# Kernel optimization log

Hardware: AMD Instinct MI355X
Metric: run time of the kernel (lower is better)

Reference implementation:

```python
import jax, jax.numpy as jnp
import numpy as np

D = 384        # model dim
H = 6          # heads
HD = 64        # head dim (inner_dim = H*HD = 384)
DEPTH = 12
P = 16         # patch size
G = 14         # grid side (224/16)
NP = G * G     # 196 patches
NC = 1000
B = 64
DFF = 4 * D
SCALE = HD ** -0.5
EPS = 1e-5


def _ln(x, w, b):
    m = x.mean(-1, keepdims=True)
    v = ((x - m) ** 2).mean(-1, keepdims=True)
    return (x - m) * jax.lax.rsqrt(v + EPS) * w + b


def setup_inputs() -> dict:
    key = jax.random.key(0)
    ks = jax.random.split(key, 16)
    s = 0.02
    inp = {
        "x": jax.random.normal(ks[0], (B, 3, 224, 224), jnp.float32),
        # patch embedding conv as matmul: weight [3*P*P, D]
        "W_patch": jax.random.normal(ks[1], (3 * P * P, D), jnp.float32) * s,
        "b_patch": jnp.zeros((D,), jnp.float32),
        "ln0_w": jnp.ones((D,), jnp.float32),
        "ln0_b": jnp.zeros((D,), jnp.float32),
        "pos_emb": jax.random.normal(ks[2], (1, NP + 1, D), jnp.float32) * s,
        "cls_token": jax.random.normal(ks[3], (1, D), jnp.float32),
        # per-block params stacked over depth
        "ln1_w": jnp.ones((DEPTH, D), jnp.float32),
        "ln1_b": jnp.zeros((DEPTH, D), jnp.float32),
        "Wq": jax.random.normal(ks[4], (DEPTH, D, H * HD), jnp.float32) * s,
        "Wkv": jax.random.normal(ks[5], (DEPTH, D, 2 * H * HD), jnp.float32) * s,
        "Wo": jax.random.normal(ks[6], (DEPTH, H * HD, D), jnp.float32) * s,
        "bo": jnp.zeros((DEPTH, D), jnp.float32),
        "ln2_w": jnp.ones((DEPTH, D), jnp.float32),
        "ln2_b": jnp.zeros((DEPTH, D), jnp.float32),
        "W1": jax.random.normal(ks[7], (DEPTH, D, DFF), jnp.float32) * s,
        "b1": jnp.zeros((DEPTH, DFF), jnp.float32),
        "W2": jax.random.normal(ks[8], (DEPTH, DFF, D), jnp.float32) * s,
        "b2": jnp.zeros((DEPTH, D), jnp.float32),
        "lnf_w": jnp.ones((D,), jnp.float32),
        "lnf_b": jnp.zeros((D,), jnp.float32),
        "Whead": jax.random.normal(ks[9], (D, NC), jnp.float32) * s,
        "bhead": jnp.zeros((NC,), jnp.float32),
    }
    return inp


def reference(x, W_patch, b_patch, ln0_w, ln0_b, pos_emb, cls_token,
              ln1_w, ln1_b, Wq, Wkv, Wo, bo, ln2_w, ln2_b,
              W1, b1, W2, b2, lnf_w, lnf_b, Whead, bhead):
    b = x.shape[0]
    # patch embed: Conv2d(3, D, P, stride=P) == extract patches + matmul
    patches = x.reshape(b, 3, G, P, G, P).transpose(0, 2, 4, 1, 3, 5).reshape(b, NP, 3 * P * P)
    h = patches @ W_patch + b_patch                     # [b, NP, D]
    h = _ln(h, ln0_w, ln0_b)
    cls = jnp.broadcast_to(cls_token[None], (b, 1, D))
    h = jnp.concatenate([cls, h], axis=1) + pos_emb     # [b, NP+1, D]
    n = NP + 1
    for d in range(DEPTH):
        # self-attention with pre-LN, residual
        a = _ln(h, ln1_w[d], ln1_b[d])
        q = (a @ Wq[d]).reshape(b, n, H, HD).transpose(0, 2, 1, 3)
        kv = a @ Wkv[d]
        k = kv[..., : H * HD].reshape(b, n, H, HD).transpose(0, 2, 1, 3)
        v = kv[..., H * HD:].reshape(b, n, H, HD).transpose(0, 2, 1, 3)
        sim = jnp.einsum('bhid,bhjd->bhij', q, k) * SCALE
        attn = jax.nn.softmax(sim, axis=-1)
        o = jnp.einsum('bhij,bhjd->bhid', attn, v)
        o = o.transpose(0, 2, 1, 3).reshape(b, n, H * HD)
        h = h + o @ Wo[d] + bo[d]
        # MLP with pre-LN, residual, exact GELU
        m = _ln(h, ln2_w[d], ln2_b[d])
        m = jax.nn.gelu(m @ W1[d] + b1[d], approximate=False)
        h = h + m @ W2[d] + b2[d]
    cls_out = h[:, 0, :]
    logits = _ln(cls_out, lnf_w, lnf_b) @ Whead + bhead
    return logits
```

## Files before the change

### kernel.cpp

```cpp
#include <hip/hip_runtime.h>


typedef unsigned short u16;
typedef __attribute__((ext_vector_type(8))) short short8;
typedef __attribute__((ext_vector_type(4))) float f32x4;
typedef __attribute__((ext_vector_type(4))) unsigned short u16x4;
typedef __attribute__((ext_vector_type(2))) unsigned short u16x2;

#define D_      384
#define NH      6
#define DEPTH_  12
#define NP_     196
#define NT_     197
#define B_      64
#define DFF_    1536
#define M_REAL  (B_*NT_)
#define M_PAD   12672
#define M_PATCH (B_*NP_)

__device__ __forceinline__ float bf2f(u16 u){
  unsigned int i = ((unsigned int)u) << 16;
  return __builtin_bit_cast(float, i);
}
__device__ __forceinline__ u16 f2bf(float f){
  unsigned int i = __builtin_bit_cast(unsigned int, f);
  i = (i + 0x7FFFu + ((i >> 16) & 1u)) >> 16;
  return (u16)i;
}

#define GLOAD_LDS16(g, l) __builtin_amdgcn_global_load_lds( \
    (const __attribute__((address_space(1))) void*)(g),      \
    (__attribute__((address_space(3))) void*)(l), 16, 0, 0)

#define MFMA_BF16(a, b, c) __builtin_amdgcn_mfma_f32_16x16x32_bf16((a), (b), (c), 0, 0, 0)

__global__ __launch_bounds__(256) void transpose_cvt(const float* __restrict__ src,
                                                     u16* __restrict__ dst, int K, int N,
                                                     size_t sstride, size_t dstride)
{
  __shared__ float tile[32][33];
  src += blockIdx.z * sstride;
  dst += blockIdx.z * dstride;
  int tx = threadIdx.x, ty = threadIdx.y;
  int n0 = blockIdx.x * 32, k0 = blockIdx.y * 32;
#pragma unroll
  for (int i = 0; i < 4; ++i)
    tile[ty + i*8][tx] = src[(size_t)(k0 + ty + i*8) * N + n0 + tx];
  __syncthreads();
#pragma unroll
  for (int i = 0; i < 4; ++i)
    dst[(size_t)(n0 + ty + i*8) * K + k0 + tx] = f2bf(tile[tx][ty + i*8]);
}

__global__ __launch_bounds__(256) void patch_extract(const float* __restrict__ x,
                                                     u16* __restrict__ patches)
{
  int r = blockIdx.x;
  int b = r / NP_, p = r % NP_;
  int gy = p / 14, gx = p % 14;
  int t = threadIdx.x;
  int py = t >> 4, px = t & 15;
#pragma unroll
  for (int c = 0; c < 3; ++c){
    float v = x[(((size_t)b*3 + c)*224 + gy*16 + py)*224 + gx*16 + px];
    patches[(size_t)r*768 + c*256 + t] = f2bf(v);
  }
}

template<int MODE, int BM, int BN>
__global__ __launch_bounds__(256) void gemm_k(const u16* __restrict__ A,
                                              const u16* __restrict__ Bt,
                                              const float* __restrict__ bias,
                                              u16* __restrict__ outb,
                                              float* __restrict__ outf,
                                              int N, int K, int nbx)
{
  constexpr int MI = BM/32;
  constexpr int NJ = BN/32;
  constexpr int L  = BM/64 + BN/64;
  __shared__ u16 As[3*BM*32];
  __shared__ u16 Bs[3*BN*32];
  int tid = threadIdx.x;
  int w = tid >> 6, lane = tid & 63;

  int nwg = gridDim.x;
  int q = nwg >> 3, r = nwg & 7;
  int xcd = blockIdx.x & 7, slot = blockIdx.x >> 3;
  int wgid = (xcd < r ? xcd*(q+1) : r*(q+1) + (xcd - r)*q) + slot;
  int m0 = (wgid / nbx) * BM;
  int n0 = (wgid % nbx) * BN;
  int wr = w >> 1, wc = w & 1;

  f32x4 acc[MI][NJ];
#pragma unroll
  for (int i = 0; i < MI; ++i)
#pragma unroll
    for (int j = 0; j < NJ; ++j) acc[i][j] = (f32x4){0.f,0.f,0.f,0.f};

  int srow = lane >> 2;
  int skc  = ((lane & 3) ^ (srow & 3)) * 8;
  const u16* Ag = A  + (size_t)(m0 + w*16 + srow) * K + skc;
  const u16* Bg = Bt + (size_t)(n0 + w*16 + srow) * K + skc;

  int fr  = lane & 15;
  int fsw = ((lane >> 4) ^ (lane & 3)) << 3;

  auto stage = [&](int bi, int kt){
    u16* Ad = As + bi*(BM*32) + (w*16)*32;
    u16* Bd = Bs + bi*(BN*32) + (w*16)*32;
#pragma unroll
    for (int c = 0; c < BM/64; ++c)
      GLOAD_LDS16(Ag + (size_t)(c*64)*K + kt, Ad + c*64*32);
#pragma unroll
    for (int c = 0; c < BN/64; ++c)
      GLOAD_LDS16(Bg + (size_t)(c*64)*K + kt, Bd + c*64*32);
  };
  auto compute = [&](int bi){
    const u16* Ab = As + bi*(BM*32);
    const u16* Bb = Bs + bi*(BN*32);
    short8 af[MI], bfr[NJ];
#pragma unroll
    for (int i = 0; i < MI; ++i)
      af[i]  = *(const short8*)&Ab[(wr*(BM/2) + i*16 + fr)*32 + fsw];
#pragma unroll
    for (int j = 0; j < NJ; ++j)
      bfr[j] = *(const short8*)&Bb[(wc*(BN/2) + j*16 + fr)*32 + fsw];
#pragma unroll
    for (int i = 0; i < MI; ++i)
#pragma unroll
      for (int j = 0; j < NJ; ++j)
        acc[i][j] = MFMA_BF16(af[i], bfr[j], acc[i][j]);
  };

  int nk = K >> 5;
  stage(0, 0);
  stage(1, 32);
  int bi = 0;
  for (int t = 0; t < nk - 1; ++t){
    __builtin_amdgcn_sched_barrier(0);
    if constexpr (L == 2) asm volatile("s_waitcnt vmcnt(2)" ::: "memory");
    else                  asm volatile("s_waitcnt vmcnt(3)" ::: "memory");
    __builtin_amdgcn_s_barrier();
    asm volatile("" ::: "memory");
    compute(bi);
    if (t + 2 < nk){
      int bs = bi + 2; if (bs >= 3) bs -= 3;
      stage(bs, (t + 2) * 32);
    }
    bi = (bi == 2) ? 0 : bi + 1;
  }
  __builtin_amdgcn_sched_barrier(0);
  asm volatile("s_waitcnt vmcnt(0)" ::: "memory");
  __builtin_amdgcn_s_barrier();
  asm volatile("" ::: "memory");
  compute(bi);

  int cr = (lane >> 4) << 2;
  int cc = lane & 15;
#pragma unroll
  for (int j = 0; j < NJ; ++j){
    int c = n0 + wc*(BN/2) + j*16 + cc;
    float bv = bias ? bias[c] : 0.f;
#pragma unroll
    for (int i = 0; i < MI; ++i){
      int rbase = m0 + wr*(BM/2) + i*16 + cr;
#pragma unroll
      for (int e = 0; e < 4; ++e){
        float v = acc[i][j][e] + bv;
        size_t idx = (size_t)(rbase + e) * N + c;
        if (MODE == 0)      outb[idx] = f2bf(v);
        else if (MODE == 1) outf[idx] += v;
        else {
          float g = 0.5f * v * (1.f + erff(v * 0.70710678118654752f));
          outb[idx] = f2bf(g);
        }
      }
    }
  }
}

__global__ __launch_bounds__(256) void ln_rows(const float* __restrict__ in,
                                               const float* __restrict__ gw,
                                               const float* __restrict__ gb,
                                               u16* __restrict__ out, int rows)
{
  int m = blockIdx.x * 4 + (threadIdx.x >> 6);
  int lane = threadIdx.x & 63;
  if (m >= rows) return;
  const float* r = in + (size_t)m * D_;
  float4 v0 = *(const float4*)(r + lane*4);
  float2 v1 = *(const float2*)(r + 256 + lane*2);
  float sum = v0.x+v0.y+v0.z+v0.w+v1.x+v1.y;
  float sq  = v0.x*v0.x+v0.y*v0.y+v0.z*v0.z+v0.w*v0.w+v1.x*v1.x+v1.y*v1.y;
#pragma unroll
  for (int d = 1; d < 64; d <<= 1){ sum += __shfl_xor(sum, d); sq += __shfl_xor(sq, d); }
  float mean = sum * (1.f/D_);
  float rs = rsqrtf(sq*(1.f/D_) - mean*mean + 1e-5f);
  float4 w0 = *(const float4*)(gw + lane*4);
  float2 w1 = *(const float2*)(gw + 256 + lane*2);
  float4 b0 = *(const float4*)(gb + lane*4);
  float2 b1v= *(const float2*)(gb + 256 + lane*2);
  u16x4 o4 = { f2bf((v0.x-mean)*rs*w0.x + b0.x), f2bf((v0.y-mean)*rs*w0.y + b0.y),
               f2bf((v0.z-mean)*rs*w0.z + b0.z), f2bf((v0.w-mean)*rs*w0.w + b0.w) };
  u16x2 o2 = { f2bf((v1.x-mean)*rs*w1.x + b1v.x), f2bf((v1.y-mean)*rs*w1.y + b1v.y) };
  *(u16x4*)(out + (size_t)m*D_ + lane*4) = o4;
  *(u16x2*)(out + (size_t)m*D_ + 256 + lane*2) = o2;
}

__global__ __launch_bounds__(256) void assemble_h(const u16* __restrict__ pe,
                                                  const float* __restrict__ gw,
                                                  const float* __restrict__ gb,
                                                  const float* __restrict__ pos,
                                                  const float* __restrict__ cls,
                                                  float* __restrict__ h)
{
  int m = blockIdx.x * 4 + (threadIdx.x >> 6);
  int lane = threadIdx.x & 63;
  if (m >= M_PAD) return;
  float* ho = h + (size_t)m * D_;
  if (m >= M_REAL){
    float4 z = {0.f,0.f,0.f,0.f};
    *(float4*)(ho + lane*4) = z;
    float2 z2 = {0.f,0.f};
    *(float2*)(ho + 256 + lane*2) = z2;
    return;
  }
  int b = m / NT_, t = m % NT_;
  const float* pr = pos + (size_t)t * D_;
  float4 p0 = *(const float4*)(pr + lane*4);
  float2 p1 = *(const float2*)(pr + 256 + lane*2);
  if (t == 0){
    float4 c0 = *(const float4*)(cls + lane*4);
    float2 c1 = *(const float2*)(cls + 256 + lane*2);
    float4 r0 = {c0.x+p0.x, c0.y+p0.y, c0.z+p0.z, c0.w+p0.w};
    float2 r1 = {c1.x+p1.x, c1.y+p1.y};
    *(float4*)(ho + lane*4) = r0;
    *(float2*)(ho + 256 + lane*2) = r1;
  } else {
    const u16* per = pe + (size_t)(b*NP_ + (t-1)) * D_;
    u16x4 a0 = *(const u16x4*)(per + lane*4);
    u16x2 a1 = *(const u16x2*)(per + 256 + lane*2);
    float x0=bf2f(a0.x), x1=bf2f(a0.y), x2=bf2f(a0.z), x3=bf2f(a0.w), x4=bf2f(a1.x), x5=bf2f(a1.y);
    float sum = x0+x1+x2+x3+x4+x5;
    float sq  = x0*x0+x1*x1+x2*x2+x3*x3+x4*x4+x5*x5;
#pragma unroll
    for (int d = 1; d < 64; d <<= 1){ sum += __shfl_xor(sum, d); sq += __shfl_xor(sq, d); }
    float mean = sum * (1.f/D_);
    float rs = rsqrtf(sq*(1.f/D_) - mean*mean + 1e-5f);
    float4 w0 = *(const float4*)(gw + lane*4);
    float2 w1 = *(const float2*)(gw + 256 + lane*2);
    float4 b0 = *(const float4*)(gb + lane*4);
    float2 b1v= *(const float2*)(gb + 256 + lane*2);
    float4 r0 = { (x0-mean)*rs*w0.x + b0.x + p0.x, (x1-mean)*rs*w0.y + b0.y + p0.y,
                  (x2-mean)*rs*w0.z + b0.z + p0.z, (x3-mean)*rs*w0.w + b0.w + p0.w };
    float2 r1 = { (x4-mean)*rs*w1.x + b1v.x + p1.x, (x5-mean)*rs*w1.y + b1v.y + p1.y };
    *(float4*)(ho + lane*4) = r0;
    *(float2*)(ho + 256 + lane*2) = r1;
  }
}

__global__ __launch_bounds__(256) void attn_k(const u16* __restrict__ qkv,
                                              u16* __restrict__ o)
{
  __shared__ u16 Ks[208*72];
  __shared__ u16 Vt[64*232];
  __shared__ u16 Ps[4][16*40];
  int bh = blockIdx.x;
  int b = bh / NH, hh = bh % NH;
  int tid = threadIdx.x, w = tid >> 6, lane = tid & 63;
  const u16* kbase = qkv + (size_t)b*NT_*1152 + 384 + hh*64;
  const u16* vbase = kbase + 384;

  int jr = tid >> 3, col = (tid & 7) * 8;
#pragma unroll
  for (int it = 0; it < 7; ++it){
    int j = it*32 + jr;
    if (j < 208){
      uint4 val = {0u,0u,0u,0u};
      if (j < 197) val = *(const uint4*)(kbase + (size_t)j*1152 + col);
      *(uint4*)&Ks[j*72 + col] = val;
    }
  }
#pragma unroll
  for (int it = 0; it < 7; ++it){
    int j = it*32 + jr;
    union { uint4 v; u16 s[8]; } u;
    u.v.x = 0u; u.v.y = 0u; u.v.z = 0u; u.v.w = 0u;
    if (j < 197) u.v = *(const uint4*)(vbase + (size_t)j*1152 + col);
#pragma unroll
    for (int e = 0; e < 8; ++e) Vt[(size_t)(col+e)*232 + j] = u.s[e];
  }
  __syncthreads();

  u16* myP = Ps[w];
  int fr = lane & 15, fk = lane >> 4;

  for (int qt = w; qt < 13; qt += 4){
    const u16* qrow = qkv + (size_t)(b*NT_ + qt*16 + fr)*1152 + hh*64 + fk*8;
    short8 aq0 = *(const short8*)qrow;
    short8 aq1 = *(const short8*)(qrow + 32);

    f32x4 s[13];
#pragma unroll
    for (int jt = 0; jt < 13; ++jt){
      const u16* kr = &Ks[(jt*16 + fr)*72 + fk*8];
      short8 bk0 = *(const short8*)kr;
      short8 bk1 = *(const short8*)(kr + 32);
      f32x4 z = {0.f,0.f,0.f,0.f};
      z = MFMA_BF16(aq0, bk0, z);
      z = MFMA_BF16(aq1, bk1, z);
      s[jt] = z;
    }

#pragma unroll
    for (int e = 0; e < 4; ++e){
      float mx = -1e30f;
#pragma unroll
      for (int jt = 0; jt < 13; ++jt){
        int cj = jt*16 + fr;
        float v = (cj < NT_) ? s[jt][e]*0.125f : -1e30f;
        s[jt][e] = v;
        mx = fmaxf(mx, v);
      }
#pragma unroll
      for (int d = 1; d < 16; d <<= 1) mx = fmaxf(mx, __shfl_xor(mx, d));
      float su = 0.f;
#pragma unroll
      for (int jt = 0; jt < 13; ++jt){
        float p = __expf(s[jt][e] - mx);
        s[jt][e] = p; su += p;
      }
#pragma unroll
      for (int d = 1; d < 16; d <<= 1) su += __shfl_xor(su, d);
      float ri = 1.f / su;
#pragma unroll
      for (int jt = 0; jt < 13; ++jt) s[jt][e] *= ri;
    }

    f32x4 oacc[4];
#pragma unroll
    for (int dt = 0; dt < 4; ++dt) oacc[dt] = (f32x4){0.f,0.f,0.f,0.f};
#pragma unroll
    for (int jc = 0; jc < 7; ++jc){
#pragma unroll
      for (int jtl = 0; jtl < 2; ++jtl){
        int jt = jc*2 + jtl;
#pragma unroll
        for (int e = 0; e < 4; ++e){
          u16 pv = 0;
          if (jt < 13) pv = f2bf(s[jt][e]);
          myP[(fk*4 + e)*40 + jtl*16 + fr] = pv;
        }
      }
      asm volatile("s_waitcnt lgkmcnt(0)" ::: "memory");
      short8 pa = *(const short8*)&myP[fr*40 + fk*8];
#pragma unroll
      for (int dt = 0; dt < 4; ++dt){
        short8 bv = *(const short8*)&Vt[(size_t)(dt*16 + fr)*232 + jc*32 + fk*8];
        oacc[dt] = MFMA_BF16(pa, bv, oacc[dt]);
      }
    }

#pragma unroll
    for (int dt = 0; dt < 4; ++dt)
#pragma unroll
      for (int e = 0; e < 4; ++e){
        int t = qt*16 + fk*4 + e;
        if (t < NT_)
          o[(size_t)(b*NT_ + t)*384 + hh*64 + dt*16 + fr] = f2bf(oacc[dt][e]);
      }
  }
}

__global__ __launch_bounds__(256) void head_k(const float* __restrict__ h,
                                              const float* __restrict__ lw,
                                              const float* __restrict__ lb,
                                              const float* __restrict__ Wh,
                                              const float* __restrict__ bh,
                                              float* __restrict__ out)
{
  __shared__ float sn[D_];
  __shared__ float red[2][4];
  int b = blockIdx.x;
  int tid = threadIdx.x;
  const float* r = h + (size_t)b * NT_ * D_;
  float x0 = r[tid];
  float x1 = (tid < 128) ? r[256 + tid] : 0.f;
  float sum = x0 + x1;
  float sq  = x0*x0 + x1*x1;
  int lane = tid & 63, w = tid >> 6;
#pragma unroll
  for (int d = 1; d < 64; d <<= 1){ sum += __shfl_xor(sum, d); sq += __shfl_xor(sq, d); }
  if (lane == 0){ red[0][w] = sum; red[1][w] = sq; }
  __syncthreads();
  sum = red[0][0]+red[0][1]+red[0][2]+red[0][3];
  sq  = red[1][0]+red[1][1]+red[1][2]+red[1][3];
  float mean = sum * (1.f/D_);
  float rs = rsqrtf(sq*(1.f/D_) - mean*mean + 1e-5f);
  sn[tid] = (x0-mean)*rs*lw[tid] + lb[tid];
  if (tid < 128) sn[256+tid] = (x1-mean)*rs*lw[256+tid] + lb[256+tid];
  __syncthreads();
  int n = blockIdx.y * 256 + tid;
  if (n < 1000){
    float acc = bh[n];
#pragma unroll 4
    for (int k = 0; k < D_; ++k) acc += sn[k] * Wh[(size_t)k*1000 + n];
    out[(size_t)b*1000 + n] = acc;
  }
}

extern "C" void kernel_launch(void* const* d_in, const int* in_sizes, int n_in,
                              void* d_out, int out_size, void* d_ws, size_t ws_size,
                              hipStream_t stream)
{
  (void)in_sizes; (void)n_in; (void)out_size; (void)ws_size;
  const float* x_in    = (const float*)d_in[0];
  const float* W_patch = (const float*)d_in[1];
  const float* b_patch = (const float*)d_in[2];
  const float* ln0_w   = (const float*)d_in[3];
  const float* ln0_b   = (const float*)d_in[4];
  const float* pos_emb = (const float*)d_in[5];
  const float* cls_tok = (const float*)d_in[6];
  const float* ln1_w   = (const float*)d_in[7];
  const float* ln1_b   = (const float*)d_in[8];
  const float* Wq      = (const float*)d_in[9];
  const float* Wkv     = (const float*)d_in[10];
  const float* Wo      = (const float*)d_in[11];
  const float* bo      = (const float*)d_in[12];
  const float* ln2_w   = (const float*)d_in[13];
  const float* ln2_b   = (const float*)d_in[14];
  const float* W1      = (const float*)d_in[15];
  const float* b1      = (const float*)d_in[16];
  const float* W2      = (const float*)d_in[17];
  const float* b2      = (const float*)d_in[18];
  const float* lnf_w   = (const float*)d_in[19];
  const float* lnf_b   = (const float*)d_in[20];
  const float* Whead   = (const float*)d_in[21];
  const float* bhead   = (const float*)d_in[22];

  char* ws = (char*)d_ws;
  size_t off = 0;
  auto nxt = [&](size_t bytes)->char* {
    char* p = ws + off;
    off += (bytes + 255) & ~(size_t)255;
    return p;
  };
  u16*   g_buf   = (u16*)  nxt((size_t)M_PAD * DFF_ * 2);
  float* hbuf    = (float*)nxt((size_t)M_PAD * D_ * 4);
  u16*   abuf    = (u16*)  nxt((size_t)M_PAD * D_ * 2);
  u16*   qkvbuf  = (u16*)  nxt((size_t)M_PAD * 1152 * 2);
  u16*   obuf    = (u16*)  nxt((size_t)M_PAD * D_ * 2);
  u16*   wT      = (u16*)  nxt((size_t)21528576 * 2);

  u16* patches = g_buf;
  u16* pebuf   = abuf;
  u16* wpT   = wT;
  u16* wqkvT = wpT   + 294912;
  u16* woT   = wqkvT + 12*442368;
  u16* w1T   = woT   + 12*147456;
  u16* w2T   = w1T   + 12*589824;

  dim3 tpb(32, 8);
  transpose_cvt<<<dim3(12, 24, 1),  tpb, 0, stream>>>(W_patch, wpT, 768, 384, 0, 0);
  transpose_cvt<<<dim3(12, 12, 12), tpb, 0, stream>>>(Wq,  wqkvT,            384, 384,
                                                      (size_t)384*384, (size_t)1152*384);
  transpose_cvt<<<dim3(24, 12, 12), tpb, 0, stream>>>(Wkv, wqkvT + 384*384,  384, 768,
                                                      (size_t)384*768, (size_t)1152*384);
  transpose_cvt<<<dim3(12, 12, 12), tpb, 0, stream>>>(Wo,  woT, 384, 384,
                                                      (size_t)384*384, (size_t)384*384);
  transpose_cvt<<<dim3(48, 12, 12), tpb, 0, stream>>>(W1,  w1T, 384, 1536,
                                                      (size_t)384*1536, (size_t)384*1536);
  transpose_cvt<<<dim3(12, 48, 12), tpb, 0, stream>>>(W2,  w2T, 1536, 384,
                                                      (size_t)1536*384, (size_t)1536*384);

  patch_extract<<<M_PATCH, 256, 0, stream>>>(x_in, patches);
  gemm_k<0,64,64><<<6*(M_PATCH/64), 256, 0, stream>>>(patches, wpT, b_patch, pebuf, nullptr, 384, 768, 6);
  assemble_h<<<M_PAD/4, 256, 0, stream>>>(pebuf, ln0_w, ln0_b, pos_emb, cls_tok, hbuf);

  for (int d = 0; d < DEPTH_; ++d){
    ln_rows<<<M_PAD/4, 256, 0, stream>>>(hbuf, ln1_w + d*384, ln1_b + d*384, abuf, M_PAD);
    gemm_k<0,64,128><<<9*(M_PAD/64), 256, 0, stream>>>(abuf, wqkvT + (size_t)d*442368, nullptr, qkvbuf, nullptr, 1152, 384, 9);
    attn_k<<<B_*NH, 256, 0, stream>>>(qkvbuf, obuf);
    gemm_k<1,64,64><<<6*(M_PAD/64), 256, 0, stream>>>(obuf, woT + (size_t)d*147456, bo + d*384, nullptr, hbuf, 384, 384, 6);
    ln_rows<<<M_PAD/4, 256, 0, stream>>>(hbuf, ln2_w + d*384, ln2_b + d*384, abuf, M_PAD);
    gemm_k<2,64,128><<<12*(M_PAD/64), 256, 0, stream>>>(abuf, w1T + (size_t)d*589824, b1 + d*1536, g_buf, nullptr, 1536, 384, 12);
    gemm_k<1,64,64><<<6*(M_PAD/64), 256, 0, stream>>>(g_buf, w2T + (size_t)d*589824, b2 + d*384, nullptr, hbuf, 384, 1536, 6);
  }

  head_k<<<dim3(B_, 4), 256, 0, stream>>>(hbuf, lnf_w, lnf_b, Whead, bhead, (float*)d_out);
}
```

Measured before the change: 1.989 ms.

## Enlarge GEMM tiles, add split-K with atomics, run classifier head through MFMA GEMM

All transformer GEMMs move to 128x128 tiles, and the two residual-add GEMMs (Wo and W2) split K across two blockIdx.y slices that accumulate into the fp32 residual with atomic adds. The bias is added only by the first slice. The patch-embedding GEMM widens to 64x128. The scalar head kernel is replaced by an LN on the CLS rows plus a bf16 MFMA GEMM against a padded, transposed head weight. Larger tiles cut redundant operand loads and split-K restores block count on the narrow-N GEMMs. In exchange, atomics make the summation order nondeterministic and the head now rounds to bf16.

```diff
diff --git a/kernel.cpp b/kernel.cpp
--- a/kernel.cpp
+++ b/kernel.cpp
@@ -36,6 +36,7 @@
 
 __global__ __launch_bounds__(256) void transpose_cvt(const float* __restrict__ src,
                                                      u16* __restrict__ dst, int K, int N,
+                                                     int Nsrc,
                                                      size_t sstride, size_t dstride)
 {
   __shared__ float tile[32][33];
@@ -44,8 +45,11 @@
   int tx = threadIdx.x, ty = threadIdx.y;
   int n0 = blockIdx.x * 32, k0 = blockIdx.y * 32;
 #pragma unroll
-  for (int i = 0; i < 4; ++i)
-    tile[ty + i*8][tx] = src[(size_t)(k0 + ty + i*8) * N + n0 + tx];
+  for (int i = 0; i < 4; ++i){
+    float v = 0.f;
+    if (n0 + tx < Nsrc) v = src[(size_t)(k0 + ty + i*8) * Nsrc + n0 + tx];
+    tile[ty + i*8][tx] = v;
+  }
   __syncthreads();
 #pragma unroll
   for (int i = 0; i < 4; ++i)
@@ -67,7 +71,7 @@
   }
 }
 
-template<int MODE, int BM, int BN>
+template<int MODE, int BM, int BN, int KS>
 __global__ __launch_bounds__(256) void gemm_k(const u16* __restrict__ A,
                                               const u16* __restrict__ Bt,
                                               const float* __restrict__ bias,
@@ -89,6 +93,9 @@
   int wgid = (xcd < r ? xcd*(q+1) : r*(q+1) + (xcd - r)*q) + slot;
   int m0 = (wgid / nbx) * BM;
   int n0 = (wgid % nbx) * BN;
+  int kz = (KS > 1) ? blockIdx.y : 0;
+  int Kl = K / KS;
+  int koff = kz * Kl;
   int wr = w >> 1, wc = w & 1;
 
   f32x4 acc[MI][NJ];
@@ -99,8 +106,8 @@
 
   int srow = lane >> 2;
   int skc  = ((lane & 3) ^ (srow & 3)) * 8;
-  const u16* Ag = A  + (size_t)(m0 + w*16 + srow) * K + skc;
-  const u16* Bg = Bt + (size_t)(n0 + w*16 + srow) * K + skc;
+  const u16* Ag = A  + (size_t)(m0 + w*16 + srow) * K + koff + skc;
+  const u16* Bg = Bt + (size_t)(n0 + w*16 + srow) * K + koff + skc;
 
   int fr  = lane & 15;
   int fsw = ((lane >> 4) ^ (lane & 3)) << 3;
@@ -132,14 +139,15 @@
         acc[i][j] = MFMA_BF16(af[i], bfr[j], acc[i][j]);
   };
 
-  int nk = K >> 5;
+  int nk = Kl >> 5;
   stage(0, 0);
   stage(1, 32);
   int bi = 0;
   for (int t = 0; t < nk - 1; ++t){
     __builtin_amdgcn_sched_barrier(0);
-    if constexpr (L == 2) asm volatile("s_waitcnt vmcnt(2)" ::: "memory");
-    else                  asm volatile("s_waitcnt vmcnt(3)" ::: "memory");
+    if constexpr (L == 2)      asm volatile("s_waitcnt vmcnt(2)" ::: "memory");
+    else if constexpr (L == 3) asm volatile("s_waitcnt vmcnt(3)" ::: "memory");
+    else                       asm volatile("s_waitcnt vmcnt(4)" ::: "memory");
     __builtin_amdgcn_s_barrier();
     asm volatile("" ::: "memory");
     compute(bi);
@@ -160,7 +168,7 @@
 #pragma unroll
   for (int j = 0; j < NJ; ++j){
     int c = n0 + wc*(BN/2) + j*16 + cc;
-    float bv = bias ? bias[c] : 0.f;
+    float bv = (bias && kz == 0) ? bias[c] : 0.f;
 #pragma unroll
     for (int i = 0; i < MI; ++i){
       int rbase = m0 + wr*(BM/2) + i*16 + cr;
@@ -169,10 +177,12 @@
         float v = acc[i][j][e] + bv;
         size_t idx = (size_t)(rbase + e) * N + c;
         if (MODE == 0)      outb[idx] = f2bf(v);
-        else if (MODE == 1) outf[idx] += v;
-        else {
+        else if (MODE == 1) unsafeAtomicAdd(&outf[idx], v);
+        else if (MODE == 2) {
           float g = 0.5f * v * (1.f + erff(v * 0.70710678118654752f));
           outb[idx] = f2bf(g);
+        } else {
+          if (c < N) outf[idx] = v;
         }
       }
     }
@@ -182,12 +192,13 @@
 __global__ __launch_bounds__(256) void ln_rows(const float* __restrict__ in,
                                                const float* __restrict__ gw,
                                                const float* __restrict__ gb,
-                                               u16* __restrict__ out, int rows)
+                                               u16* __restrict__ out, int rows,
+                                               size_t rstride)
 {
   int m = blockIdx.x * 4 + (threadIdx.x >> 6);
   int lane = threadIdx.x & 63;
   if (m >= rows) return;
-  const float* r = in + (size_t)m * D_;
+  const float* r = in + (size_t)m * rstride;
   float4 v0 = *(const float4*)(r + lane*4);
   float2 v1 = *(const float2*)(r + 256 + lane*2);
   float sum = v0.x+v0.y+v0.z+v0.w+v1.x+v1.y;
@@ -369,43 +380,6 @@
         if (t < NT_)
           o[(size_t)(b*NT_ + t)*384 + hh*64 + dt*16 + fr] = f2bf(oacc[dt][e]);
       }
-  }
-}
-
-__global__ __launch_bounds__(256) void head_k(const float* __restrict__ h,
-                                              const float* __restrict__ lw,
-                                              const float* __restrict__ lb,
-                                              const float* __restrict__ Wh,
-                                              const float* __restrict__ bh,
-                                              float* __restrict__ out)
-{
-  __shared__ float sn[D_];
-  __shared__ float red[2][4];
-  int b = blockIdx.x;
-  int tid = threadIdx.x;
-  const float* r = h + (size_t)b * NT_ * D_;
-  float x0 = r[tid];
-  float x1 = (tid < 128) ? r[256 + tid] : 0.f;
-  float sum = x0 + x1;
-  float sq  = x0*x0 + x1*x1;
-  int lane = tid & 63, w = tid >> 6;
-#pragma unroll
-  for (int d = 1; d < 64; d <<= 1){ sum += __shfl_xor(sum, d); sq += __shfl_xor(sq, d); }
-  if (lane == 0){ red[0][w] = sum; red[1][w] = sq; }
-  __syncthreads();
-  sum = red[0][0]+red[0][1]+red[0][2]+red[0][3];
-  sq  = red[1][0]+red[1][1]+red[1][2]+red[1][3];
-  float mean = sum * (1.f/D_);
-  float rs = rsqrtf(sq*(1.f/D_) - mean*mean + 1e-5f);
-  sn[tid] = (x0-mean)*rs*lw[tid] + lb[tid];
-  if (tid < 128) sn[256+tid] = (x1-mean)*rs*lw[256+tid] + lb[256+tid];
-  __syncthreads();
-  int n = blockIdx.y * 256 + tid;
-  if (n < 1000){
-    float acc = bh[n];
-#pragma unroll 4
-    for (int k = 0; k < D_; ++k) acc += sn[k] * Wh[(size_t)k*1000 + n];
-    out[(size_t)b*1000 + n] = acc;
   }
 }
 
@@ -450,6 +424,8 @@
   u16*   abuf    = (u16*)  nxt((size_t)M_PAD * D_ * 2);
   u16*   qkvbuf  = (u16*)  nxt((size_t)M_PAD * 1152 * 2);
   u16*   obuf    = (u16*)  nxt((size_t)M_PAD * D_ * 2);
+  u16*   lncls   = (u16*)  nxt((size_t)B_ * D_ * 2);
+  u16*   whT     = (u16*)  nxt((size_t)1024 * D_ * 2);
   u16*   wT      = (u16*)  nxt((size_t)21528576 * 2);
 
   u16* patches = g_buf;
@@ -461,31 +437,33 @@
   u16* w2T   = w1T   + 12*589824;
 
   dim3 tpb(32, 8);
-  transpose_cvt<<<dim3(12, 24, 1),  tpb, 0, stream>>>(W_patch, wpT, 768, 384, 0, 0);
-  transpose_cvt<<<dim3(12, 12, 12), tpb, 0, stream>>>(Wq,  wqkvT,            384, 384,
+  transpose_cvt<<<dim3(12, 24, 1),  tpb, 0, stream>>>(W_patch, wpT, 768, 384, 384, 0, 0);
+  transpose_cvt<<<dim3(12, 12, 12), tpb, 0, stream>>>(Wq,  wqkvT,            384, 384, 384,
                                                       (size_t)384*384, (size_t)1152*384);
-  transpose_cvt<<<dim3(24, 12, 12), tpb, 0, stream>>>(Wkv, wqkvT + 384*384,  384, 768,
+  transpose_cvt<<<dim3(24, 12, 12), tpb, 0, stream>>>(Wkv, wqkvT + 384*384,  384, 768, 768,
                                                       (size_t)384*768, (size_t)1152*384);
-  transpose_cvt<<<dim3(12, 12, 12), tpb, 0, stream>>>(Wo,  woT, 384, 384,
+  transpose_cvt<<<dim3(12, 12, 12), tpb, 0, stream>>>(Wo,  woT, 384, 384, 384,
                                                       (size_t)384*384, (size_t)384*384);
-  transpose_cvt<<<dim3(48, 12, 12), tpb, 0, stream>>>(W1,  w1T, 384, 1536,
+  transpose_cvt<<<dim3(48, 12, 12), tpb, 0, stream>>>(W1,  w1T, 384, 1536, 1536,
                                                       (size_t)384*1536, (size_t)384*1536);
-  transpose_cvt<<<dim3(12, 48, 12), tpb, 0, stream>>>(W2,  w2T, 1536, 384,
+  transpose_cvt<<<dim3(12, 48, 12), tpb, 0, stream>>>(W2,  w2T, 1536, 384, 384,
                                                       (size_t)1536*384, (size_t)1536*384);
+  transpose_cvt<<<dim3(32, 12, 1),  tpb, 0, stream>>>(Whead, whT, 384, 1024, 1000, 0, 0);
 
   patch_extract<<<M_PATCH, 256, 0, stream>>>(x_in, patches);
-  gemm_k<0,64,64><<<6*(M_PATCH/64), 256, 0, stream>>>(patches, wpT, b_patch, pebuf, nullptr, 384, 768, 6);
+  gemm_k<0,64,128,1><<<3*(M_PATCH/64), 256, 0, stream>>>(patches, wpT, b_patch, pebuf, nullptr, 384, 768, 3);
   assemble_h<<<M_PAD/4, 256, 0, stream>>>(pebuf, ln0_w, ln0_b, pos_emb, cls_tok, hbuf);
 
   for (int d = 0; d < DEPTH_; ++d){
-    ln_rows<<<M_PAD/4, 256, 0, stream>>>(hbuf, ln1_w + d*384, ln1_b + d*384, abuf, M_PAD);
-    gemm_k<0,64,128><<<9*(M_PAD/64), 256, 0, stream>>>(abuf, wqkvT + (size_t)d*442368, nullptr, qkvbuf, nullptr, 1152, 384, 9);
+    ln_rows<<<M_PAD/4, 256, 0, stream>>>(hbuf, ln1_w + d*384, ln1_b + d*384, abuf, M_PAD, D_);
+    gemm_k<0,128,128,1><<<9*(M_PAD/128), 256, 0, stream>>>(abuf, wqkvT + (size_t)d*442368, nullptr, qkvbuf, nullptr, 1152, 384, 9);
     attn_k<<<B_*NH, 256, 0, stream>>>(qkvbuf, obuf);
-    gemm_k<1,64,64><<<6*(M_PAD/64), 256, 0, stream>>>(obuf, woT + (size_t)d*147456, bo + d*384, nullptr, hbuf, 384, 384, 6);
-    ln_rows<<<M_PAD/4, 256, 0, stream>>>(hbuf, ln2_w + d*384, ln2_b + d*384, abuf, M_PAD);
-    gemm_k<2,64,128><<<12*(M_PAD/64), 256, 0, stream>>>(abuf, w1T + (size_t)d*589824, b1 + d*1536, g_buf, nullptr, 1536, 384, 12);
-    gemm_k<1,64,64><<<6*(M_PAD/64), 256, 0, stream>>>(g_buf, w2T + (size_t)d*589824, b2 + d*384, nullptr, hbuf, 384, 1536, 6);
-  }
-
-  head_k<<<dim3(B_, 4), 256, 0, stream>>>(hbuf, lnf_w, lnf_b, Whead, bhead, (float*)d_out);
-}
+    gemm_k<1,128,128,2><<<dim3(3*(M_PAD/128), 2), 256, 0, stream>>>(obuf, woT + (size_t)d*147456, bo + d*384, nullptr, hbuf, 384, 384, 3);
+    ln_rows<<<M_PAD/4, 256, 0, stream>>>(hbuf, ln2_w + d*384, ln2_b + d*384, abuf, M_PAD, D_);
+    gemm_k<2,128,128,1><<<12*(M_PAD/128), 256, 0, stream>>>(abuf, w1T + (size_t)d*589824, b1 + d*1536, g_buf, nullptr, 1536, 384, 12);
+    gemm_k<1,128,128,2><<<dim3(3*(M_PAD/128), 2), 256, 0, stream>>>(g_buf, w2T + (size_t)d*589824, b2 + d*384, nullptr, hbuf, 384, 1536, 3);
+  }
+
+  ln_rows<<<B_/4, 256, 0, stream>>>(hbuf, lnf_w, lnf_b, lncls, B_, (size_t)NT_*D_);
+  gemm_k<3,64,64,1><<<16, 256, 0, stream>>>(lncls, whT, bhead, nullptr, (float*)d_out, 1000, 384, 16);
+}
```

Result: slower. 2.264 ms (+13.8%).
